# Kernel optimization log

Measured on AMD Instinct MI355X. Metric: run time of the kernel, lower is better.

The kernel has to match this reference:

```python
import jax, jax.numpy as jnp
import numpy as np

ALPHA = 0.2  # LeakyReLU negative slope

def setup_inputs() -> dict:
    key = jax.random.key(0)
    k1, k2, k3 = jax.random.split(key, 3)
    B, N, D_in, D_out = 4, 512, 512, 256
    H = jax.random.normal(k1, (B, N, D_in), dtype=jnp.float32)
    # xavier-style scaled params
    W = jax.random.normal(k2, (D_out, D_in), dtype=jnp.float32) * (2.0 / (D_in + D_out)) ** 0.5
    a = jax.random.normal(k3, (D_out, 1), dtype=jnp.float32) * (2.0 / (D_out + 1)) ** 0.5
    return {"H": H, "W": W, "a": a}

def reference(H, W, a):
    # Wh: [B, N, D_out]
    Wh = jnp.einsum('bnd,od->bno', H, W)
    # additive pairwise scores: e[b,i,j] = leakyrelu(Wh[b,i]+Wh[b,j]) . a
    e = jnp.einsum('bijo,o->bij',
                   jax.nn.leaky_relu(Wh[:, :, None, :] + Wh[:, None, :, :], ALPHA),
                   a[:, 0])
    attention = jax.nn.softmax(e, axis=-1)          # [B, N, N]
    H_att = jnp.einsum('bij,bjo->bio', attention, Wh)  # [B, N, D_out]
    return H_att
```

## Files before the change

### kernel.cpp

```cpp
#include <hip/hip_runtime.h>

constexpr int Bq   = 4;
constexpr int Nq   = 512;
constexpr int DIN  = 512;
constexpr int DOUT = 256;

typedef _Float16 h2  __attribute__((ext_vector_type(2)));
typedef _Float16 h8  __attribute__((ext_vector_type(8)));
typedef float    f4v __attribute__((ext_vector_type(4)));
typedef float    v2f __attribute__((ext_vector_type(2)));

#if defined(__has_builtin) && __has_builtin(__builtin_amdgcn_fdot2)
__device__ __forceinline__ float fdot2f(h2 a, h2 b, float c) {
    return __builtin_amdgcn_fdot2(a, b, c, false);
}
#else
__device__ __forceinline__ float fdot2f(h2 a, h2 b, float c) {
    return (float)a.x * (float)b.x + (float)a.y * (float)b.y + c;
}
#endif

__device__ __forceinline__ h8 cvt8(float4 lo, float4 hi) {
    h8 r;
    r[0] = (_Float16)lo.x; r[1] = (_Float16)lo.y;
    r[2] = (_Float16)lo.z; r[3] = (_Float16)lo.w;
    r[4] = (_Float16)hi.x; r[5] = (_Float16)hi.y;
    r[6] = (_Float16)hi.z; r[7] = (_Float16)hi.w;
    return r;
}

__global__ __launch_bounds__(256) void k1_wh(const float* __restrict__ H,
                                             const float* __restrict__ W,
                                             const float* __restrict__ a,
                                             float* __restrict__ Wh,
                                             h2* __restrict__ Wh16,
                                             h2* __restrict__ WhT16p,
                                             h2* __restrict__ a16) {
    const int bid = blockIdx.x;
    const int t   = threadIdx.x;

    if (bid == 512) {
        if (t < 64) {
            const int idx = 2 * t;
            const float4 v = *(const float4*)&a[2 * idx];
            h2 h0; h0.x = (_Float16)v.x; h0.y = (_Float16)v.y;
            h2 h1; h1.x = (_Float16)v.z; h1.y = (_Float16)v.w;
            a16[idx] = h0; a16[idx + 1] = h1;
        }
        return;
    }

    const int w    = t >> 6;
    const int lane = t & 63;
    const int mt   = bid >> 2;
    const int b    = mt & 3;
    const int n0   = (mt >> 2) << 4;
    const int o0   = ((bid & 3) << 6) + (w << 4);
    const int quad = lane >> 4;
    const int col  = lane & 15;

    const float4* __restrict__ aP =
        (const float4*)(H + (size_t)(b * Nq + n0 + col) * DIN) + quad * 2;
    const float4* __restrict__ bP =
        (const float4*)(W + (size_t)(o0 + col) * DIN) + quad * 2;

    f4v acc = {0.f, 0.f, 0.f, 0.f};
    float4 fa0 = aP[0], fa1 = aP[1];
    float4 fb0 = bP[0], fb1 = bP[1];

#pragma unroll
    for (int kb = 0; kb < 16; ++kb) {
        float4 na0 = fa0, na1 = fa1, nb0 = fb0, nb1 = fb1;
        if (kb < 15) {
            na0 = aP[(kb + 1) * 8];
            na1 = aP[(kb + 1) * 8 + 1];
            nb0 = bP[(kb + 1) * 8];
            nb1 = bP[(kb + 1) * 8 + 1];
        }
        const h8 af = cvt8(fa0, fa1);
        const h8 bf = cvt8(fb0, fb1);
        acc = __builtin_amdgcn_mfma_f32_16x16x32_f16(af, bf, acc, 0, 0, 0);
        fa0 = na0; fa1 = na1; fb0 = nb0; fb1 = nb1;
    }

    const int rowb = b * Nq + n0 + quad * 4;
#pragma unroll
    for (int reg = 0; reg < 4; ++reg) {
        const float v = acc[reg];
        Wh[(size_t)(rowb + reg) * DOUT + o0 + col] = v;
        const float vp = __shfl_xor(v, 1);
        if ((col & 1) == 0) {
            h2 hv; hv.x = (_Float16)v; hv.y = (_Float16)vp;
            const int o2 = (o0 + col) >> 1;
            Wh16[(size_t)(rowb + reg) * 128 + o2] = hv;
            WhT16p[(size_t)b * 65536 + (size_t)o2 * 512 + (n0 + quad * 4 + reg)] = hv;
        }
    }
}

__global__ __launch_bounds__(1024, 8) void k23(const float* __restrict__ Wh,
                                               const h2* __restrict__ Wh16,
                                               const h2* __restrict__ WhT16p,
                                               const h2* __restrict__ a16,
                                               float* __restrict__ out) {
    const int t   = threadIdx.x;
    const int blk = blockIdx.x;
    const int b   = blk & 3;
    const int i0  = (blk >> 2) << 2;

    __shared__ float smem[8192];
    __shared__ float sP[4 * 512];
    __shared__ float wred[2][4][8];

    {
        const int h  = __builtin_amdgcn_readfirstlane(t >> 9);
        const int j  = t & 511;
        const int ob = h * 64;

        const h2* __restrict__ wjp = WhT16p + (size_t)b * 65536 + (size_t)ob * 512 + j;
        const h2* __restrict__ wip = Wh16 + (size_t)(b * Nq + i0) * 128;

        float ab[4] = {0.f, 0.f, 0.f, 0.f};
        float rja = 0.f;
        h2 cA[8], cB[8];

#define K2_L8(buf, kb)                                                      \
    _Pragma("unroll") for (int s = 0; s < 8; ++s)                           \
        buf[s] = wjp[((kb) + s) * 512];

#define K2_C8(buf, kb)                                                      \
    _Pragma("unroll") for (int s = 0; s < 8; ++s) {                         \
        const int o2 = ob + (kb) + s;                                       \
        const h2 a2 = a16[o2];                                  \
        rja = fdot2f(a2, buf[s], rja);                                      \
        _Pragma("unroll") for (int rr = 0; rr < 4; ++rr) {                  \
            const h2 wi = wip[rr * 128 + o2];                   \
            h2 w  = buf[s] + wi;                                \
            h2 aw = __builtin_elementwise_max(w, -w);           \
            ab[rr] = fdot2f(a2, aw, ab[rr]);                    \
        }                                                                   \
    }

        K2_L8(cA, 0)  K2_L8(cB, 8)
        K2_C8(cA, 0)  K2_L8(cA, 16)
        K2_C8(cB, 8)  K2_L8(cB, 24)
        K2_C8(cA, 16) K2_L8(cA, 32)
        K2_C8(cB, 24) K2_L8(cB, 40)
        K2_C8(cA, 32) K2_L8(cA, 48)
        K2_C8(cB, 40) K2_L8(cB, 56)
        K2_C8(cA, 48)
        K2_C8(cB, 56)
#undef K2_L8
#undef K2_C8

        float* sAb = smem;
        float* sRh = smem + 2048;
        float* sRf = smem + 2560;
        if (h == 1) {
#pragma unroll
            for (int rr = 0; rr < 4; ++rr) sAb[rr * 512 + j] = ab[rr];
            sRh[j] = rja;
        }
        __syncthreads();

        float rj = 0.f;
        if (h == 0) {
#pragma unroll
            for (int rr = 0; rr < 4; ++rr) ab[rr] += sAb[rr * 512 + j];
            rj = rja + sRh[j];
            sRf[j] = rj;
        }
        __syncthreads();

        float e[4], pv[4];
        const int lane = t & 63;
        const int w    = t >> 6;

        if (h == 0) {
#pragma unroll
            for (int rr = 0; rr < 4; ++rr)
                e[rr] = 0.6f * (sRf[i0 + rr] + rj) + 0.4f * ab[rr];
#pragma unroll
            for (int rr = 0; rr < 4; ++rr) {
                float v = e[rr];
#pragma unroll
                for (int off = 32; off > 0; off >>= 1) v = fmaxf(v, __shfl_xor(v, off));
                if (lane == 0) wred[0][rr][w] = v;
            }
        }
        __syncthreads();
        if (h == 0) {
#pragma unroll
            for (int rr = 0; rr < 4; ++rr) {
                const float4 q0 = *(const float4*)&wred[0][rr][0];
                const float4 q1 = *(const float4*)&wred[0][rr][4];
                const float m = fmaxf(fmaxf(fmaxf(q0.x, q0.y), fmaxf(q0.z, q0.w)),
                                      fmaxf(fmaxf(q1.x, q1.y), fmaxf(q1.z, q1.w)));
                pv[rr] = __expf(e[rr] - m);
            }
#pragma unroll
            for (int rr = 0; rr < 4; ++rr) {
                float v = pv[rr];
#pragma unroll
                for (int off = 32; off > 0; off >>= 1) v += __shfl_xor(v, off);
                if (lane == 0) wred[1][rr][w] = v;
            }
        }
        __syncthreads();
        if (h == 0) {
#pragma unroll
            for (int rr = 0; rr < 4; ++rr) {
                const float4 q0 = *(const float4*)&wred[1][rr][0];
                const float4 q1 = *(const float4*)&wred[1][rr][4];
                const float s = (q0.x + q0.y + q0.z + q0.w) + (q1.x + q1.y + q1.z + q1.w);
                sP[rr * 512 + j] = pv[rr] * (1.0f / s);
            }
        }
        __syncthreads();
    }

    {
        const int w16 = __builtin_amdgcn_readfirstlane(t >> 6);
        const int jh  = w16 & 7;
        const int rh  = w16 >> 3;
        const int oq  = t & 63;

        const float4* __restrict__ wh4 = (const float4*)(Wh + (size_t)b * Nq * DOUT) + oq;

        v2f accL[2] = {(v2f)0.f, (v2f)0.f};
        v2f accH[2] = {(v2f)0.f, (v2f)0.f};

        const int j0 = jh * 64;
        float4 bufA[4], bufB[4];
#pragma unroll
        for (int s = 0; s < 4; ++s) bufA[s] = wh4[(j0 + s) * 64];

        for (int it = 0; it < 8; ++it) {
            const int jA = j0 + it * 8, jB = jA + 4;
#pragma unroll
            for (int s = 0; s < 4; ++s) bufB[s] = wh4[(jB + s) * 64];
#pragma unroll
            for (int rr = 0; rr < 2; ++rr) {
                const float4 p4 = *(const float4*)&sP[(rh * 2 + rr) * 512 + jA];
#pragma unroll
                for (int x = 0; x < 4; ++x) {
                    const float pj = ((const float*)&p4)[x];
                    const v2f pj2 = pj;
                    const v2f wl = {bufA[x].x, bufA[x].y};
                    const v2f wh = {bufA[x].z, bufA[x].w};
                    accL[rr] = __builtin_elementwise_fma(pj2, wl, accL[rr]);
                    accH[rr] = __builtin_elementwise_fma(pj2, wh, accH[rr]);
                }
            }
            if (it < 7) {
#pragma unroll
                for (int s = 0; s < 4; ++s) bufA[s] = wh4[(jA + 8 + s) * 64];
            }
#pragma unroll
            for (int rr = 0; rr < 2; ++rr) {
                const float4 p4 = *(const float4*)&sP[(rh * 2 + rr) * 512 + jB];
#pragma unroll
                for (int x = 0; x < 4; ++x) {
                    const float pj = ((const float*)&p4)[x];
                    const v2f pj2 = pj;
                    const v2f wl = {bufB[x].x, bufB[x].y};
                    const v2f wh = {bufB[x].z, bufB[x].w};
                    accL[rr] = __builtin_elementwise_fma(pj2, wl, accL[rr]);
                    accH[rr] = __builtin_elementwise_fma(pj2, wh, accH[rr]);
                }
            }
        }

        float4* sPart = (float4*)smem;
#pragma unroll
        for (int rr = 0; rr < 2; ++rr) {
            const int row = rh * 2 + rr;
            float4 f;
            f.x = accL[rr].x; f.y = accL[rr].y; f.z = accH[rr].x; f.w = accH[rr].y;
            sPart[(jh * 4 + row) * 64 + oq] = f;
        }
        __syncthreads();

        if (t < 256) {
            const int row = t >> 6, oqq = t & 63;
            float4 fin = make_float4(0.f, 0.f, 0.f, 0.f);
#pragma unroll
            for (int j8 = 0; j8 < 8; ++j8) {
                const float4 v = sPart[(j8 * 4 + row) * 64 + oqq];
                fin.x += v.x; fin.y += v.y; fin.z += v.z; fin.w += v.w;
            }
            ((float4*)(out + ((size_t)(b * Nq) + i0 + row) * DOUT))[oqq] = fin;
        }
    }
}

extern "C" void kernel_launch(void* const* d_in, const int* in_sizes, int n_in,
                              void* d_out, int out_size, void* d_ws, size_t ws_size,
                              hipStream_t stream) {
    const float* H = (const float*)d_in[0];
    const float* W = (const float*)d_in[1];
    const float* a = (const float*)d_in[2];
    float* out = (float*)d_out;

    float* Wh  = (float*)d_ws;
    h2* Wh16   = (h2*)(Wh + 524288);
    h2* WhT16p = Wh16 + 262144;
    h2* a16    = WhT16p + 262144;

    hipLaunchKernelGGL(k1_wh, dim3(513), dim3(256),  0, stream, H, W, a, Wh, Wh16, WhT16p, a16);
    hipLaunchKernelGGL(k23,   dim3(512), dim3(1024), 0, stream, Wh, Wh16, WhT16p, a16, out);
}
```

Before: 109.4 us.

## Restructure P·Wh accumulation so each wave covers all four rows

The final attention-times-Wh stage changes its work split. Before, each wave handled 2 rows over 64 j values. Now each of the 16 waves handles all 4 rows over 32 j values, so every Wh float4 loaded from global memory is reused across 4 rows instead of 2, roughly halving global Wh traffic. The cross-wave reduction becomes two-stage: waves 8-15 write partials to shared memory, waves 0-7 add theirs in, and 256 threads sum the remaining 8 slices. The explicit software double-buffering of Wh loads is removed in favour of unroll 2. There are more accumulator registers and one extra barrier.

```diff
diff --git a/kernel.cpp b/kernel.cpp
--- a/kernel.cpp
+++ b/kernel.cpp
@@ -221,75 +221,70 @@
 
     {
         const int w16 = __builtin_amdgcn_readfirstlane(t >> 6);
-        const int jh  = w16 & 7;
-        const int rh  = w16 >> 3;
         const int oq  = t & 63;
+        const int jb  = w16 * 32;
 
         const float4* __restrict__ wh4 = (const float4*)(Wh + (size_t)b * Nq * DOUT) + oq;
 
-        v2f accL[2] = {(v2f)0.f, (v2f)0.f};
-        v2f accH[2] = {(v2f)0.f, (v2f)0.f};
-
-        const int j0 = jh * 64;
-        float4 bufA[4], bufB[4];
-#pragma unroll
-        for (int s = 0; s < 4; ++s) bufA[s] = wh4[(j0 + s) * 64];
-
-        for (int it = 0; it < 8; ++it) {
-            const int jA = j0 + it * 8, jB = jA + 4;
-#pragma unroll
-            for (int s = 0; s < 4; ++s) bufB[s] = wh4[(jB + s) * 64];
-#pragma unroll
-            for (int rr = 0; rr < 2; ++rr) {
-                const float4 p4 = *(const float4*)&sP[(rh * 2 + rr) * 512 + jA];
-#pragma unroll
-                for (int x = 0; x < 4; ++x) {
-                    const float pj = ((const float*)&p4)[x];
-                    const v2f pj2 = pj;
-                    const v2f wl = {bufA[x].x, bufA[x].y};
-                    const v2f wh = {bufA[x].z, bufA[x].w};
-                    accL[rr] = __builtin_elementwise_fma(pj2, wl, accL[rr]);
-                    accH[rr] = __builtin_elementwise_fma(pj2, wh, accH[rr]);
-                }
-            }
-            if (it < 7) {
-#pragma unroll
-                for (int s = 0; s < 4; ++s) bufA[s] = wh4[(jA + 8 + s) * 64];
-            }
-#pragma unroll
-            for (int rr = 0; rr < 2; ++rr) {
-                const float4 p4 = *(const float4*)&sP[(rh * 2 + rr) * 512 + jB];
-#pragma unroll
-                for (int x = 0; x < 4; ++x) {
-                    const float pj = ((const float*)&p4)[x];
-                    const v2f pj2 = pj;
-                    const v2f wl = {bufB[x].x, bufB[x].y};
-                    const v2f wh = {bufB[x].z, bufB[x].w};
-                    accL[rr] = __builtin_elementwise_fma(pj2, wl, accL[rr]);
-                    accH[rr] = __builtin_elementwise_fma(pj2, wh, accH[rr]);
-                }
+        f4v acc[4];
+#pragma unroll
+        for (int rr = 0; rr < 4; ++rr) acc[rr] = (f4v)0.f;
+
+#pragma unroll 2
+        for (int s = 0; s < 8; ++s) {
+            const int j = jb + s * 4;
+            const float4 w0 = wh4[(j + 0) * 64];
+            const float4 w1 = wh4[(j + 1) * 64];
+            const float4 w2 = wh4[(j + 2) * 64];
+            const float4 w3 = wh4[(j + 3) * 64];
+            const f4v v0 = {w0.x, w0.y, w0.z, w0.w};
+            const f4v v1 = {w1.x, w1.y, w1.z, w1.w};
+            const f4v v2 = {w2.x, w2.y, w2.z, w2.w};
+            const f4v v3 = {w3.x, w3.y, w3.z, w3.w};
+#pragma unroll
+            for (int rr = 0; rr < 4; ++rr) {
+                const float4 p4 = *(const float4*)&sP[rr * 512 + j];
+                acc[rr] = __builtin_elementwise_fma((f4v)p4.x, v0, acc[rr]);
+                acc[rr] = __builtin_elementwise_fma((f4v)p4.y, v1, acc[rr]);
+                acc[rr] = __builtin_elementwise_fma((f4v)p4.z, v2, acc[rr]);
+                acc[rr] = __builtin_elementwise_fma((f4v)p4.w, v3, acc[rr]);
             }
         }
 
         float4* sPart = (float4*)smem;
-#pragma unroll
-        for (int rr = 0; rr < 2; ++rr) {
-            const int row = rh * 2 + rr;
-            float4 f;
-            f.x = accL[rr].x; f.y = accL[rr].y; f.z = accH[rr].x; f.w = accH[rr].y;
-            sPart[(jh * 4 + row) * 64 + oq] = f;
+        if (w16 >= 8) {
+#pragma unroll
+            for (int rr = 0; rr < 4; ++rr) {
+                float4 f;
+                f.x = acc[rr][0]; f.y = acc[rr][1]; f.z = acc[rr][2]; f.w = acc[rr][3];
+                sPart[((w16 - 8) * 4 + rr) * 64 + oq] = f;
+            }
+        }
+        __syncthreads();
+        if (w16 < 8) {
+#pragma unroll
+            for (int rr = 0; rr < 4; ++rr) {
+                const int idx = (w16 * 4 + rr) * 64 + oq;
+                const float4 v = sPart[idx];
+                float4 f;
+                f.x = acc[rr][0] + v.x; f.y = acc[rr][1] + v.y;
+                f.z = acc[rr][2] + v.z; f.w = acc[rr][3] + v.w;
+                sPart[idx] = f;
+            }
         }
         __syncthreads();
 
         if (t < 256) {
             const int row = t >> 6, oqq = t & 63;
-            float4 fin = make_float4(0.f, 0.f, 0.f, 0.f);
-#pragma unroll
-            for (int j8 = 0; j8 < 8; ++j8) {
-                const float4 v = sPart[(j8 * 4 + row) * 64 + oqq];
-                fin.x += v.x; fin.y += v.y; fin.z += v.z; fin.w += v.w;
-            }
-            ((float4*)(out + ((size_t)(b * Nq) + i0 + row) * DOUT))[oqq] = fin;
+            f4v fin = (f4v)0.f;
+#pragma unroll
+            for (int k = 0; k < 8; ++k) {
+                const float4 v = sPart[(k * 4 + row) * 64 + oqq];
+                fin[0] += v.x; fin[1] += v.y; fin[2] += v.z; fin[3] += v.w;
+            }
+            float4 f;
+            f.x = fin[0]; f.y = fin[1]; f.z = fin[2]; f.w = fin[3];
+            ((float4*)(out + ((size_t)(b * Nq) + i0 + row) * DOUT))[oqq] = f;
         }
     }
 }
```

New measurement: 101.9 us. 6.8% less time.
